# Kernel tuning notes

Measured on AMD Instinct MI355X. Metric: run time of the kernel, lower is better.

## Reference

```python
import jax, jax.numpy as jnp
import numpy as np

E, I, D = 8, 2816, 1024   # num_experts, intermediate_size, dim
T, A = 1024, 2            # tokens, top-k experts per token


def setup_inputs() -> dict:
    key = jax.random.key(0)
    k1, k2, k3, k4, k5 = jax.random.split(key, 5)
    x = jax.random.normal(k1, (T, D), dtype=jnp.float32)
    expert_indices = jax.random.randint(k2, (T, A), 0, E, dtype=jnp.int64)
    scale = 0.02
    w1 = jax.random.normal(k3, (E, I, D), dtype=jnp.float32) * scale
    w2 = jax.random.normal(k4, (E, D, I), dtype=jnp.float32) * scale
    w3 = jax.random.normal(k5, (E, I, D), dtype=jnp.float32) * scale
    return {"x": x, "w1": w1, "w2": w2, "w3": w3, "expert_indices": expert_indices}


def reference(x, w1, w2, w3, expert_indices):
    # x: [T, D], expert_indices: [T, A]
    # Same math as torch: silu(x @ w1[e].T) * (x @ w3[e].T) @ w2[e].T per (t, a).
    # Compute all-expert projections once, then gather the selected expert rows
    # (avoids materializing the [T, A, I, D] per-token weight copies).
    idx = expert_indices.astype(jnp.int32)
    h1 = jnp.einsum('ti,eoi->teo', x, w1)              # [T, E, I]
    h3 = jnp.einsum('ti,eoi->teo', x, w3)              # [T, E, I]
    g1 = jnp.take_along_axis(h1, idx[:, :, None], axis=1)  # [T, A, I]
    g3 = jnp.take_along_axis(h3, idx[:, :, None], axis=1)  # [T, A, I]
    h = jax.nn.silu(g1) * g3                            # SwiGLU, [T, A, I]
    y_all = jnp.einsum('tao,eio->taei', h, w2)          # [T, A, E, D]
    out = jnp.take_along_axis(y_all, idx[:, :, None, None], axis=2)  # [T, A, 1, D]
    return out[:, :, 0, :]                              # [T, A, D]
```

## Files before the change

kernel.cpp:

```cpp
#include <hip/hip_runtime.h>
#include <hip/hip_bf16.h>

#define E_NUM 8
#define I_DIM 2816
#define D_DIM 1024
#define T_NUM 1024
#define A_TOP 2
#define NPAIR (T_NUM * A_TOP)
#define PADROWS 3072
#define MT_MAX (PADROWS / 128)
#define KSPLIT 4
#define KCHUNK (I_DIM / KSPLIT)
#define KT2 (KCHUNK / 32)

#define HB_OFF    16384ULL
#define HB_BYTES  ((unsigned long long)PADROWS * I_DIM * 2ULL)
#define XBF_OFF   (HB_OFF + HB_BYTES)

typedef __bf16 bf16x8 __attribute__((ext_vector_type(8)));
typedef float  f32x4  __attribute__((ext_vector_type(4)));

__device__ inline unsigned pk2(float a, float b) {
  __hip_bfloat162 h = __float22bfloat162_rn(make_float2(a, b));
  union { __hip_bfloat162 h; unsigned u; } c; c.h = h; return c.u;
}
__device__ inline uint4 pack8(float4 a, float4 b) {
  return make_uint4(pk2(a.x, a.y), pk2(a.z, a.w), pk2(b.x, b.y), pk2(b.z, b.w));
}
__device__ inline unsigned short f2bf(float f) {
  __hip_bfloat16 h = __float2bfloat16(f);
  union { __hip_bfloat16 h; unsigned short u; } c; c.h = h; return c.u;
}
__device__ inline void gload_lds16(const unsigned short* g, unsigned short* l) {
  __builtin_amdgcn_global_load_lds((const __attribute__((address_space(1))) void*)g,
                                   (__attribute__((address_space(3))) void*)l, 16, 0, 0);
}

__global__ __launch_bounds__(256) void sort_pairs_kernel(
    const int* __restrict__ eidx, int* __restrict__ meta, int* __restrict__ pairs)
{
  __shared__ int cnt[E_NUM];
  __shared__ int pstart[E_NUM + 1];
  __shared__ int cur[E_NUM];
  int tid = threadIdx.x;
  if (tid < E_NUM) cnt[tid] = 0;
  __syncthreads();
  for (int p = tid; p < NPAIR; p += 256) atomicAdd(&cnt[eidx[p] & 7], 1);
  for (int i = tid; i < PADROWS; i += 256) pairs[i] = -1;
  __syncthreads();
  if (tid == 0) {
    int s = 0;
    for (int e = 0; e < E_NUM; ++e) {
      pstart[e] = s; cur[e] = s;
      s += ((cnt[e] + 127) / 128) * 128;
    }
    pstart[E_NUM] = s;
  }
  __syncthreads();
  for (int p = tid; p < NPAIR; p += 256) {
    int e = eidx[p] & 7;
    int pos = atomicAdd(&cur[e], 1);
    pairs[pos] = p;
  }
  __syncthreads();
  if (tid <= E_NUM) meta[tid] = pstart[tid];
}

__global__ __launch_bounds__(256) void convertx_kernel(
    const float* __restrict__ in, unsigned short* __restrict__ out)
{
  size_t i = (size_t)(blockIdx.x * 256 + threadIdx.x) * 8;
  const float4* p = (const float4*)(in + i);
  *(uint4*)(out + i) = pack8(p[0], p[1]);
}

__global__ __launch_bounds__(256, 4) void stage1_v5(
    const unsigned short* __restrict__ xbf, const float* __restrict__ w1,
    const float* __restrict__ w3, const int* __restrict__ meta,
    const int* __restrict__ pairs, unsigned short* __restrict__ hbuf)
{
  int mtile = blockIdx.y;
  if (mtile * 128 >= meta[E_NUM]) return;
  int e = 0;
  while (meta[e + 1] <= mtile * 128) ++e;
  int ntile = blockIdx.x;

  __shared__ alignas(16) unsigned short As[2][128 * 32];
  __shared__ alignas(16) unsigned short B1s[2][64 * 32];
  __shared__ alignas(16) unsigned short B3s[2][64 * 32];
  __shared__ int rowtok[128];

  int tid = threadIdx.x;
  for (int i = tid; i < 128; i += 256) {
    int p = pairs[mtile * 128 + i];
    rowtok[i] = (p >= 0) ? (p >> 1) : -1;
  }
  __syncthreads();

  int lane = tid & 63, w = tid >> 6;
  int wm = w >> 1, wn = w & 1, lrow = lane & 15, quad = lane >> 4;

  size_t axoff[2];
#pragma unroll
  for (int j = 0; j < 2; ++j) {
    int r = 32 * w + 16 * j + (lane >> 2);
    int tok = rowtok[r]; if (tok < 0) tok = 0;
    axoff[j] = (size_t)tok * D_DIM + (lane & 3) * 8;
  }
  const float* pw1 = w1 + ((size_t)e * I_DIM + ntile * 64 + (tid >> 2)) * D_DIM + (tid & 3) * 8;
  const float* pw3 = w3 + ((size_t)e * I_DIM + ntile * 64 + (tid >> 2)) * D_DIM + (tid & 3) * 8;
  int bws = (tid >> 2) * 32 + (tid & 3) * 8;

  f32x4 acc1[4][2], acc3[4][2];
#pragma unroll
  for (int i = 0; i < 4; ++i)
#pragma unroll
    for (int j = 0; j < 2; ++j) {
      acc1[i][j] = (f32x4){0.f, 0.f, 0.f, 0.f};
      acc3[i][j] = (f32x4){0.f, 0.f, 0.f, 0.f};
    }

  float4 r1[2], r3[2];
  r1[0] = *(const float4*)(pw1);     r1[1] = *(const float4*)(pw1 + 4);
  r3[0] = *(const float4*)(pw3);     r3[1] = *(const float4*)(pw3 + 4);
  gload_lds16(xbf + axoff[0], &As[0][(32 * w) * 32]);
  gload_lds16(xbf + axoff[1], &As[0][(32 * w + 16) * 32]);
  *(uint4*)&B1s[0][bws] = pack8(r1[0], r1[1]);
  *(uint4*)&B3s[0][bws] = pack8(r3[0], r3[1]);

  const int KT = D_DIM / 32;
  for (int k = 0; k < KT; ++k) {
    __syncthreads();
    int kk = k & 1;
    if (k + 1 < KT) {
      int kn = (k + 1) * 32;
      r1[0] = *(const float4*)(pw1 + kn); r1[1] = *(const float4*)(pw1 + kn + 4);
      r3[0] = *(const float4*)(pw3 + kn); r3[1] = *(const float4*)(pw3 + kn + 4);
      gload_lds16(xbf + axoff[0] + kn, &As[kk ^ 1][(32 * w) * 32]);
      gload_lds16(xbf + axoff[1] + kn, &As[kk ^ 1][(32 * w + 16) * 32]);
    }
    bf16x8 af[4];
#pragma unroll
    for (int mi = 0; mi < 4; ++mi)
      af[mi] = *(const bf16x8*)&As[kk][(wm * 64 + mi * 16 + lrow) * 32 + quad * 8];
#pragma unroll
    for (int ni = 0; ni < 2; ++ni) {
      bf16x8 b1 = *(const bf16x8*)&B1s[kk][(wn * 32 + ni * 16 + lrow) * 32 + quad * 8];
#pragma unroll
      for (int mi = 0; mi < 4; ++mi)
        acc1[mi][ni] = __builtin_amdgcn_mfma_f32_16x16x32_bf16(af[mi], b1, acc1[mi][ni], 0, 0, 0);
      bf16x8 b3 = *(const bf16x8*)&B3s[kk][(wn * 32 + ni * 16 + lrow) * 32 + quad * 8];
#pragma unroll
      for (int mi = 0; mi < 4; ++mi)
        acc3[mi][ni] = __builtin_amdgcn_mfma_f32_16x16x32_bf16(af[mi], b3, acc3[mi][ni], 0, 0, 0);
    }
    if (k + 1 < KT) {
      *(uint4*)&B1s[kk ^ 1][bws] = pack8(r1[0], r1[1]);
      *(uint4*)&B3s[kk ^ 1][bws] = pack8(r3[0], r3[1]);
    }
  }

#pragma unroll
  for (int mi = 0; mi < 4; ++mi) {
#pragma unroll
    for (int r = 0; r < 4; ++r) {
      int lr = wm * 64 + mi * 16 + quad * 4 + r;
      if (rowtok[lr] >= 0) {
        size_t base = (size_t)(mtile * 128 + lr) * I_DIM + (size_t)ntile * 64 + wn * 32;
#pragma unroll
        for (int ni = 0; ni < 2; ++ni) {
          float v1 = acc1[mi][ni][r];
          float v3 = acc3[mi][ni][r];
          float hv = (v1 / (1.f + __expf(-v1))) * v3;
          hbuf[base + ni * 16 + lrow] = f2bf(hv);
        }
      }
    }
  }
}

__global__ __launch_bounds__(256, 4) void stage2_v5(
    const unsigned short* __restrict__ hbuf, const float* __restrict__ w2,
    const int* __restrict__ meta, const int* __restrict__ pairs,
    float* __restrict__ out)
{
  int mtile = blockIdx.y;
  if (mtile * 128 >= meta[E_NUM]) return;
  int e = 0;
  while (meta[e + 1] <= mtile * 128) ++e;
  int ntile = blockIdx.x;
  int kbase = blockIdx.z * KCHUNK;

  __shared__ alignas(16) unsigned short As[2][128 * 32];
  __shared__ alignas(16) unsigned short Bs[2][128 * 32];
  __shared__ int prow[128];

  int tid = threadIdx.x;
  for (int i = tid; i < 128; i += 256) prow[i] = pairs[mtile * 128 + i];
  __syncthreads();

  int lane = tid & 63, w = tid >> 6;
  int wm = w >> 1, wn = w & 1, lrow = lane & 15, quad = lane >> 4;

  size_t axoff[2];
#pragma unroll
  for (int j = 0; j < 2; ++j) {
    int r = 32 * w + 16 * j + (lane >> 2);
    axoff[j] = (size_t)(mtile * 128 + r) * I_DIM + kbase + (lane & 3) * 8;
  }
  const float* pw2[2];
  int bws[2];
#pragma unroll
  for (int j = 0; j < 2; ++j) {
    int row = j * 64 + (tid >> 2);
    pw2[j] = w2 + ((size_t)e * D_DIM + ntile * 128 + row) * I_DIM + kbase + (tid & 3) * 8;
    bws[j] = row * 32 + (tid & 3) * 8;
  }

  f32x4 acc[4][4];
#pragma unroll
  for (int i = 0; i < 4; ++i)
#pragma unroll
    for (int j = 0; j < 4; ++j) acc[i][j] = (f32x4){0.f, 0.f, 0.f, 0.f};

  float4 rb[2][2];
#pragma unroll
  for (int j = 0; j < 2; ++j) {
    rb[j][0] = *(const float4*)(pw2[j]);
    rb[j][1] = *(const float4*)(pw2[j] + 4);
    gload_lds16(hbuf + axoff[j], &As[0][(32 * w + 16 * j) * 32]);
  }
#pragma unroll
  for (int j = 0; j < 2; ++j)
    *(uint4*)&Bs[0][bws[j]] = pack8(rb[j][0], rb[j][1]);

  for (int k = 0; k < KT2; ++k) {
    __syncthreads();
    int kk = k & 1;
    if (k + 1 < KT2) {
      int kn = (k + 1) * 32;
#pragma unroll
      for (int j = 0; j < 2; ++j) {
        rb[j][0] = *(const float4*)(pw2[j] + kn);
        rb[j][1] = *(const float4*)(pw2[j] + kn + 4);
        gload_lds16(hbuf + axoff[j] + kn, &As[kk ^ 1][(32 * w + 16 * j) * 32]);
      }
    }
    bf16x8 af[4];
#pragma unroll
    for (int mi = 0; mi < 4; ++mi)
      af[mi] = *(const bf16x8*)&As[kk][(wm * 64 + mi * 16 + lrow) * 32 + quad * 8];
#pragma unroll
    for (int ni = 0; ni < 4; ++ni) {
      bf16x8 bfr = *(const bf16x8*)&Bs[kk][(wn * 64 + ni * 16 + lrow) * 32 + quad * 8];
#pragma unroll
      for (int mi = 0; mi < 4; ++mi)
        acc[mi][ni] = __builtin_amdgcn_mfma_f32_16x16x32_bf16(af[mi], bfr, acc[mi][ni], 0, 0, 0);
    }
    if (k + 1 < KT2) {
#pragma unroll
      for (int j = 0; j < 2; ++j)
        *(uint4*)&Bs[kk ^ 1][bws[j]] = pack8(rb[j][0], rb[j][1]);
    }
  }

#pragma unroll
  for (int mi = 0; mi < 4; ++mi) {
#pragma unroll
    for (int r = 0; r < 4; ++r) {
      int lr = wm * 64 + mi * 16 + quad * 4 + r;
      int p = prow[lr];
      if (p >= 0) {
        float* obase = out + (size_t)p * D_DIM + (size_t)ntile * 128 + wn * 64;
#pragma unroll
        for (int ni = 0; ni < 4; ++ni)
          atomicAdd(obase + ni * 16 + lrow, acc[mi][ni][r]);
      }
    }
  }
}

extern "C" void kernel_launch(void* const* d_in, const int* in_sizes, int n_in,
                              void* d_out, int out_size, void* d_ws, size_t ws_size,
                              hipStream_t stream) {
  const float* x  = (const float*)d_in[0];
  const float* w1 = (const float*)d_in[1];
  const float* w2 = (const float*)d_in[2];
  const float* w3 = (const float*)d_in[3];
  const int* eidx = (const int*)d_in[4];
  float* out = (float*)d_out;

  int* meta  = (int*)d_ws;
  int* pairs = (int*)((char*)d_ws + 64);
  unsigned short* hbuf = (unsigned short*)((char*)d_ws + HB_OFF);
  unsigned short* xbf  = (unsigned short*)((char*)d_ws + XBF_OFF);

  sort_pairs_kernel<<<1, 256, 0, stream>>>(eidx, meta, pairs);
  convertx_kernel<<<(T_NUM * D_DIM) / 8 / 256, 256, 0, stream>>>(x, xbf);
  hipMemsetAsync(out, 0, (size_t)out_size * sizeof(float), stream);

  dim3 g1(I_DIM / 64, MT_MAX);
  stage1_v5<<<g1, 256, 0, stream>>>(xbf, w1, w3, meta, pairs, hbuf);
  dim3 g2(D_DIM / 128, MT_MAX, KSPLIT);
  stage2_v5<<<g2, 256, 0, stream>>>(hbuf, w2, meta, pairs, out);
}
```

Measured before the change: 337.5 us.

## Fuse prep kernels, remap blocks for XCD locality, raise stage2 K-split

Merges the sort, x-to-bf16 conversion and output zeroing into one prep kernel, which removes two launches and a memset. Both GEMM stages remap block IDs so that blocks sharing the same weight tiles are grouped per XCD, assuming round-robin dispatch across the 8 dies, to improve L2 reuse. Stage2 now splits K 8 ways instead of 4, which gives more parallelism at the cost of twice the atomic adds on the output.

```diff
diff --git a/kernel.cpp b/kernel.cpp
--- a/kernel.cpp
+++ b/kernel.cpp
@@ -9,7 +9,7 @@
 #define NPAIR (T_NUM * A_TOP)
 #define PADROWS 3072
 #define MT_MAX (PADROWS / 128)
-#define KSPLIT 4
+#define KSPLIT 8
 #define KCHUNK (I_DIM / KSPLIT)
 #define KT2 (KCHUNK / 32)
 
@@ -36,54 +36,62 @@
                                    (__attribute__((address_space(3))) void*)l, 16, 0, 0);
 }
 
-__global__ __launch_bounds__(256) void sort_pairs_kernel(
-    const int* __restrict__ eidx, int* __restrict__ meta, int* __restrict__ pairs)
+__global__ __launch_bounds__(256) void prep_kernel(
+    const int* __restrict__ eidx, const float* __restrict__ x,
+    int* __restrict__ meta, int* __restrict__ pairs,
+    unsigned short* __restrict__ xbf, float* __restrict__ out)
 {
-  __shared__ int cnt[E_NUM];
-  __shared__ int pstart[E_NUM + 1];
-  __shared__ int cur[E_NUM];
+  int bid = blockIdx.x;
   int tid = threadIdx.x;
-  if (tid < E_NUM) cnt[tid] = 0;
-  __syncthreads();
-  for (int p = tid; p < NPAIR; p += 256) atomicAdd(&cnt[eidx[p] & 7], 1);
-  for (int i = tid; i < PADROWS; i += 256) pairs[i] = -1;
-  __syncthreads();
-  if (tid == 0) {
-    int s = 0;
-    for (int e = 0; e < E_NUM; ++e) {
-      pstart[e] = s; cur[e] = s;
-      s += ((cnt[e] + 127) / 128) * 128;
-    }
-    pstart[E_NUM] = s;
-  }
-  __syncthreads();
-  for (int p = tid; p < NPAIR; p += 256) {
-    int e = eidx[p] & 7;
-    int pos = atomicAdd(&cur[e], 1);
-    pairs[pos] = p;
-  }
-  __syncthreads();
-  if (tid <= E_NUM) meta[tid] = pstart[tid];
-}
-
-__global__ __launch_bounds__(256) void convertx_kernel(
-    const float* __restrict__ in, unsigned short* __restrict__ out)
-{
-  size_t i = (size_t)(blockIdx.x * 256 + threadIdx.x) * 8;
-  const float4* p = (const float4*)(in + i);
-  *(uint4*)(out + i) = pack8(p[0], p[1]);
-}
-
-__global__ __launch_bounds__(256, 4) void stage1_v5(
+  if (bid == 0) {
+    __shared__ int cnt[E_NUM];
+    __shared__ int pstart[E_NUM + 1];
+    __shared__ int cur[E_NUM];
+    if (tid < E_NUM) cnt[tid] = 0;
+    __syncthreads();
+    for (int p = tid; p < NPAIR; p += 256) atomicAdd(&cnt[eidx[p] & 7], 1);
+    for (int i = tid; i < PADROWS; i += 256) pairs[i] = -1;
+    __syncthreads();
+    if (tid == 0) {
+      int s = 0;
+      for (int e = 0; e < E_NUM; ++e) {
+        pstart[e] = s; cur[e] = s;
+        s += ((cnt[e] + 127) / 128) * 128;
+      }
+      pstart[E_NUM] = s;
+    }
+    __syncthreads();
+    for (int p = tid; p < NPAIR; p += 256) {
+      int e = eidx[p] & 7;
+      int pos = atomicAdd(&cur[e], 1);
+      pairs[pos] = p;
+    }
+    __syncthreads();
+    if (tid <= E_NUM) meta[tid] = pstart[tid];
+  } else if (bid <= 512) {
+    size_t i = (size_t)((bid - 1) * 256 + tid) * 8;
+    const float4* p = (const float4*)(x + i);
+    *(uint4*)(xbf + i) = pack8(p[0], p[1]);
+  } else {
+    uint4 z = make_uint4(0u, 0u, 0u, 0u);
+    uint4* po = (uint4*)out + (size_t)(bid - 513) * 1024 + tid;
+#pragma unroll
+    for (int k = 0; k < 4; ++k) po[k * 256] = z;
+  }
+}
+
+__global__ __launch_bounds__(256, 4) void stage1_v8(
     const unsigned short* __restrict__ xbf, const float* __restrict__ w1,
     const float* __restrict__ w3, const int* __restrict__ meta,
     const int* __restrict__ pairs, unsigned short* __restrict__ hbuf)
 {
-  int mtile = blockIdx.y;
+  int orig = blockIdx.x + 44 * blockIdx.y;
+  int nid  = (orig & 7) * 132 + (orig >> 3);
+  int ntile = nid / MT_MAX;
+  int mtile = nid % MT_MAX;
   if (mtile * 128 >= meta[E_NUM]) return;
   int e = 0;
   while (meta[e + 1] <= mtile * 128) ++e;
-  int ntile = blockIdx.x;
 
   __shared__ alignas(16) unsigned short As[2][128 * 32];
   __shared__ alignas(16) unsigned short B1s[2][64 * 32];
@@ -179,17 +187,21 @@
   }
 }
 
-__global__ __launch_bounds__(256, 4) void stage2_v5(
+__global__ __launch_bounds__(256, 4) void stage2_v8(
     const unsigned short* __restrict__ hbuf, const float* __restrict__ w2,
     const int* __restrict__ meta, const int* __restrict__ pairs,
     float* __restrict__ out)
 {
-  int mtile = blockIdx.y;
+  int orig = blockIdx.x + 8 * (blockIdx.y + MT_MAX * blockIdx.z);
+  int nid  = (orig & 7) * 192 + (orig >> 3);
+  int mtile = nid % MT_MAX;
+  int rest  = nid / MT_MAX;
+  int ntile = rest & 7;
+  int kc    = rest >> 3;
   if (mtile * 128 >= meta[E_NUM]) return;
   int e = 0;
   while (meta[e + 1] <= mtile * 128) ++e;
-  int ntile = blockIdx.x;
-  int kbase = blockIdx.z * KCHUNK;
+  int kbase = kc * KCHUNK;
 
   __shared__ alignas(16) unsigned short As[2][128 * 32];
   __shared__ alignas(16) unsigned short Bs[2][128 * 32];
@@ -295,12 +307,10 @@
   unsigned short* hbuf = (unsigned short*)((char*)d_ws + HB_OFF);
   unsigned short* xbf  = (unsigned short*)((char*)d_ws + XBF_OFF);
 
-  sort_pairs_kernel<<<1, 256, 0, stream>>>(eidx, meta, pairs);
-  convertx_kernel<<<(T_NUM * D_DIM) / 8 / 256, 256, 0, stream>>>(x, xbf);
-  hipMemsetAsync(out, 0, (size_t)out_size * sizeof(float), stream);
+  prep_kernel<<<641, 256, 0, stream>>>(eidx, x, meta, pairs, xbf, out);
 
   dim3 g1(I_DIM / 64, MT_MAX);
-  stage1_v5<<<g1, 256, 0, stream>>>(xbf, w1, w3, meta, pairs, hbuf);
+  stage1_v8<<<g1, 256, 0, stream>>>(xbf, w1, w3, meta, pairs, hbuf);
   dim3 g2(D_DIM / 128, MT_MAX, KSPLIT);
-  stage2_v5<<<g2, 256, 0, stream>>>(hbuf, w2, meta, pairs, out);
-}
+  stage2_v8<<<g2, 256, 0, stream>>>(hbuf, w2, meta, pairs, out);
+}
```

After: 391.1 us. +15.9%, slower.
